# Kernel tuning notes

Measured on AMD Instinct MI355X. Metric: run time of the kernel, lower is better.

Reference implementation:

```python
import jax, jax.numpy as jnp
import numpy as np
import math

B, T, C, H, RANK, RD = 8, 512, 2048, 16, 8, 16
HD = C // H  # 128
ADAPTER_SCALE = 1.0 / RANK  # scale / rank with scale=1.0


def setup_inputs() -> dict:
    key = jax.random.key(0)
    ks = jax.random.split(key, 7)
    x = jax.random.normal(ks[0], (B, T, C), dtype=jnp.float32)
    # frozen random linears (weights ~ N(0,1)/sqrt(in_features))
    Wqkv = jax.random.normal(ks[1], (3 * C, C), dtype=jnp.float32) / math.sqrt(C)
    Wout = jax.random.normal(ks[2], (C, C), dtype=jnp.float32) / math.sqrt(C)
    # VeRA frozen random matrices
    A0_qkv = jax.random.normal(ks[3], (RANK, C), dtype=jnp.float32) / math.sqrt(C)
    B0_qkv = jax.random.normal(ks[4], (3 * C, RANK), dtype=jnp.float32) / math.sqrt(RANK)
    A0_out = jax.random.normal(ks[5], (RANK, C), dtype=jnp.float32) / math.sqrt(C)
    B0_out = jax.random.normal(ks[6], (C, RANK), dtype=jnp.float32) / math.sqrt(RANK)
    # learned scaling vectors (init to ones, as in the module)
    d_a_qkv = jnp.ones((RANK,), dtype=jnp.float32)
    d_b_qkv = jnp.ones((RANK,), dtype=jnp.float32)
    d_a_out = jnp.ones((RANK,), dtype=jnp.float32)
    d_b_out = jnp.ones((RANK,), dtype=jnp.float32)
    # partial RoPE caches over first RD dims
    freqs = 1.0 / (10000.0 ** (jnp.arange(0, RD, 2, dtype=jnp.float32) / RD))  # [RD/2]
    ang = jnp.arange(T, dtype=jnp.float32)[:, None] * freqs[None, :]  # [T, RD/2]
    cos = jnp.cos(ang)
    sin = jnp.sin(ang)
    return {"x": x, "Wqkv": Wqkv, "A0_qkv": A0_qkv, "B0_qkv": B0_qkv,
            "d_a_qkv": d_a_qkv, "d_b_qkv": d_b_qkv,
            "Wout": Wout, "A0_out": A0_out, "B0_out": B0_out,
            "d_a_out": d_a_out, "d_b_out": d_b_out,
            "cos": cos, "sin": sin}


def _adapted_linear(x, W, A0, B0, d_a, d_b):
    # frozen(x) + VeRA adapter: diag(d_b) B0 diag(d_a) A0, scaled by 1/rank
    base = x @ W.T
    h = (x @ A0.T) * (d_a * d_b)
    return base + (h @ B0.T) * ADAPTER_SCALE


def _apply_rope(q, cos, sin):
    # q: [B, H, T, HD]; rotate first RD dims, pass-through the rest
    x_rope, x_pass = q[..., :RD], q[..., RD:]
    half = RD // 2
    x1, x2 = x_rope[..., :half], x_rope[..., half:]
    c = cos[None, None]  # [1,1,T,RD/2]
    s = sin[None, None]
    rot = jnp.concatenate([x1 * c - x2 * s, x2 * c + x1 * s], axis=-1)
    return jnp.concatenate([rot, x_pass], axis=-1)


def reference(x, Wqkv, A0_qkv, B0_qkv, d_a_qkv, d_b_qkv,
              Wout, A0_out, B0_out, d_a_out, d_b_out, cos, sin):
    qkv = _adapted_linear(x, Wqkv, A0_qkv, B0_qkv, d_a_qkv, d_b_qkv)  # [B,T,3C]
    qkv = qkv.reshape(B, T, 3, H, HD)
    q = jnp.transpose(qkv[:, :, 0], (0, 2, 1, 3))  # [B,H,T,HD]
    k = jnp.transpose(qkv[:, :, 1], (0, 2, 1, 3))
    v = jnp.transpose(qkv[:, :, 2], (0, 2, 1, 3))
    q = _apply_rope(q, cos, sin)
    k = _apply_rope(k, cos, sin)
    # causal SDPA
    scale = 1.0 / math.sqrt(HD)
    scores = jnp.einsum('bhqd,bhkd->bhqk', q, k) * scale
    mask = jnp.tril(jnp.ones((T, T), dtype=bool))
    scores = jnp.where(mask[None, None], scores, jnp.finfo(scores.dtype).min)
    attn = jax.nn.softmax(scores, axis=-1)
    y = jnp.einsum('bhqk,bhkd->bhqd', attn, v)  # [B,H,T,HD]
    y = jnp.transpose(y, (0, 2, 1, 3)).reshape(B, T, C)
    return _adapted_linear(y, Wout, A0_out, B0_out, d_a_out, d_b_out)
```

## Files before the change

kernel.cpp:

```cpp
#include <hip/hip_runtime.h>

typedef unsigned short ushort_t;
typedef __attribute__((ext_vector_type(8))) short short8;
typedef __attribute__((ext_vector_type(4))) float f32x4;

#define AS1(p) ((const __attribute__((address_space(1))) void*)(p))
#define AS3(p) ((__attribute__((address_space(3))) void*)(p))

__device__ __forceinline__ ushort_t f2bf(float f){
  unsigned u = __float_as_uint(f);
  u += 0x7FFFu + ((u>>16)&1u);
  return (ushort_t)(u>>16);
}
__device__ __forceinline__ float bf2f(ushort_t h){
  return __uint_as_float(((unsigned)h)<<16);
}

__global__ __launch_bounds__(256) void conv_f2b(const float* __restrict__ src,
                                                ushort_t* __restrict__ dst, int n){
  int i = (blockIdx.x*256 + threadIdx.x)*4;
  if (i < n){
    float4 v = *(const float4*)&src[i];
    ushort_t o0=f2bf(v.x), o1=f2bf(v.y), o2=f2bf(v.z), o3=f2bf(v.w);
    ushort4 o; o.x=o0; o.y=o1; o.z=o2; o.w=o3;
    *(ushort4*)&dst[i] = o;
  }
}

__global__ __launch_bounds__(256) void lora_h_f32(const float* __restrict__ X,
                                                  ushort_t* __restrict__ Xbf,
                                                  const float* __restrict__ A0,
                                                  const float* __restrict__ da,
                                                  const float* __restrict__ db,
                                                  float* __restrict__ out, int K){
  int m = blockIdx.x;
  int tid = threadIdx.x, lane = tid & 63, w = tid >> 6;
  float part[8] = {0,0,0,0,0,0,0,0};
  for (int k = tid; k < K; k += 256){
    float xv = X[(size_t)m*K + k];
    Xbf[(size_t)m*K + k] = f2bf(xv);
    #pragma unroll
    for (int r=0;r<8;++r) part[r] += xv * A0[r*K + k];
  }
  #pragma unroll
  for (int r=0;r<8;++r)
    for (int d=1;d<64;d<<=1) part[r] += __shfl_xor(part[r], d, 64);
  __shared__ float wsum[4][8];
  if (lane==0){
    #pragma unroll
    for (int r=0;r<8;++r) wsum[w][r] = part[r];
  }
  __syncthreads();
  if (tid < 8){
    float s = wsum[0][tid]+wsum[1][tid]+wsum[2][tid]+wsum[3][tid];
    out[(size_t)m*8 + tid] = s * da[tid]*db[tid];
  }
}

__global__ __launch_bounds__(256) void lora_h_bf16(const ushort_t* __restrict__ X,
                                                   const float* __restrict__ A0,
                                                   const float* __restrict__ da,
                                                   const float* __restrict__ db,
                                                   float* __restrict__ out, int K){
  int m = blockIdx.x;
  int tid = threadIdx.x, lane = tid & 63, w = tid >> 6;
  float part[8] = {0,0,0,0,0,0,0,0};
  for (int k = tid; k < K; k += 256){
    float xv = bf2f(X[(size_t)m*K + k]);
    #pragma unroll
    for (int r=0;r<8;++r) part[r] += xv * A0[r*K + k];
  }
  #pragma unroll
  for (int r=0;r<8;++r)
    for (int d=1;d<64;d<<=1) part[r] += __shfl_xor(part[r], d, 64);
  __shared__ float wsum[4][8];
  if (lane==0){
    #pragma unroll
    for (int r=0;r<8;++r) wsum[w][r] = part[r];
  }
  __syncthreads();
  if (tid < 8){
    float s = wsum[0][tid]+wsum[1][tid]+wsum[2][tid]+wsum[3][tid];
    out[(size_t)m*8 + tid] = s * da[tid]*db[tid];
  }
}

__global__ __launch_bounds__(512, 1) void gemm256x192_lora(
    const ushort_t* __restrict__ A, const ushort_t* __restrict__ Bw,
    const float* __restrict__ hmat, const float* __restrict__ B0,
    ushort_t* __restrict__ C, int M, int N, int K)
{
  __shared__ __align__(16) char smem[114688];
  const int tid = threadIdx.x, lane = tid & 63, w = tid >> 6;
  const int wm = w >> 1, wn = w & 1;

  const int nbn = N / 192;
  const int nwg = (M >> 8) * nbn;
  const int q8 = nwg >> 3;
  const int swz = ((int)blockIdx.x & 7)*q8 + ((int)blockIdx.x >> 3);
  const int m0 = (swz / nbn) << 8, n0 = (swz % nbn) * 192;

  const int NTt = K >> 6;
  const int srow8  = tid >> 3;
  const int schunk = (lane & 7) ^ (lane >> 3);

  #define STAGE_AU(u, tt, bb) do { \
    const ushort_t* g_ = A + (size_t)(m0 + (u)*64 + srow8)*K + (tt)*64 + schunk*8; \
    __builtin_amdgcn_global_load_lds(AS1(g_), AS3(smem + (bb)*32768 + (u)*8192 + tid*16), 16, 0, 0); \
  } while(0)
  #define STAGE_BU(u, tt, bb) do { \
    const ushort_t* g_ = Bw + (size_t)(n0 + (u)*64 + srow8)*K + (tt)*64 + schunk*8; \
    __builtin_amdgcn_global_load_lds(AS1(g_), AS3(smem + 65536 + (bb)*24576 + (u)*8192 + tid*16), 16, 0, 0); \
  } while(0)

  #define RDA(bb, q, kk) (*(const short8*)(smem + (bb)*32768 + \
      ((q)*64 + wm*16 + (lane&15))*128 + ((((kk)*4 + (lane>>4)) ^ (lane&7))<<4)))
  #define RDB(bb, r, kk) (*(const short8*)(smem + 65536 + (bb)*24576 + \
      ((r)*32 + wn*16 + (lane&15))*128 + ((((kk)*4 + (lane>>4)) ^ (lane&7))<<4)))

  #define MM(q, r, bi) do{ \
    acc[q][r] = __builtin_amdgcn_mfma_f32_16x16x32_bf16(aF[q][0], bF[bi][0], acc[q][r], 0,0,0); \
    acc[q][r] = __builtin_amdgcn_mfma_f32_16x16x32_bf16(aF[q][1], bF[bi][1], acc[q][r], 0,0,0); \
  }while(0)

  #define BARRIER() asm volatile("s_barrier" ::: "memory")

  short8 aF[4][2];
  short8 bF[2][2];
  f32x4 acc[4][6] = {};

  STAGE_AU(0,0,0); STAGE_AU(1,0,0); STAGE_AU(2,0,0); STAGE_AU(3,0,0);
  STAGE_BU(0,0,0); STAGE_BU(1,0,0); STAGE_BU(2,0,0);
  asm volatile("s_waitcnt vmcnt(2)" ::: "memory");
  BARRIER();

  for (int t = 0; t < NTt-1; ++t){
    const int b = t & 1, nb = b ^ 1;
    #pragma unroll
    for (int q=0;q<4;++q){ aF[q][0]=RDA(b,q,0); aF[q][1]=RDA(b,q,1); }
    #pragma unroll
    for (int rl=0;rl<2;++rl){ bF[rl][0]=RDB(b,rl,0); bF[rl][1]=RDB(b,rl,1); }
    STAGE_AU(0,t+1,nb); STAGE_AU(1,t+1,nb);
    __builtin_amdgcn_s_setprio(1);
    MM(0,0,0); MM(0,1,1); MM(1,0,0); MM(1,1,1);
    MM(2,0,0); MM(2,1,1); MM(3,0,0); MM(3,1,1);
    __builtin_amdgcn_s_setprio(0);
    asm volatile("s_waitcnt vmcnt(3)" ::: "memory");
    BARRIER();
    #pragma unroll
    for (int rl=0;rl<2;++rl){ bF[rl][0]=RDB(b,rl+2,0); bF[rl][1]=RDB(b,rl+2,1); }
    STAGE_AU(2,t+1,nb); STAGE_AU(3,t+1,nb); STAGE_BU(0,t+1,nb);
    __builtin_amdgcn_s_setprio(1);
    MM(0,2,0); MM(0,3,1); MM(1,2,0); MM(1,3,1);
    MM(2,2,0); MM(2,3,1); MM(3,2,0); MM(3,3,1);
    __builtin_amdgcn_s_setprio(0);
    asm volatile("s_waitcnt vmcnt(5)" ::: "memory");
    BARRIER();
    #pragma unroll
    for (int rl=0;rl<2;++rl){ bF[rl][0]=RDB(b,rl+4,0); bF[rl][1]=RDB(b,rl+4,1); }
    STAGE_BU(1,t+1,nb); STAGE_BU(2,t+1,nb);
    __builtin_amdgcn_s_setprio(1);
    MM(0,4,0); MM(0,5,1); MM(1,4,0); MM(1,5,1);
    MM(2,4,0); MM(2,5,1); MM(3,4,0); MM(3,5,1);
    __builtin_amdgcn_s_setprio(0);
    asm volatile("s_waitcnt lgkmcnt(0)" ::: "memory");
    asm volatile("s_waitcnt vmcnt(2)" ::: "memory");
    BARRIER();
  }

  {
    const int b = (NTt-1) & 1;
    #pragma unroll
    for (int q=0;q<4;++q){ aF[q][0]=RDA(b,q,0); aF[q][1]=RDA(b,q,1); }
    #pragma unroll
    for (int rl=0;rl<2;++rl){ bF[rl][0]=RDB(b,rl,0); bF[rl][1]=RDB(b,rl,1); }
    __builtin_amdgcn_s_setprio(1);
    MM(0,0,0); MM(0,1,1); MM(1,0,0); MM(1,1,1);
    MM(2,0,0); MM(2,1,1); MM(3,0,0); MM(3,1,1);
    __builtin_amdgcn_s_setprio(0);
    asm volatile("s_waitcnt vmcnt(1)" ::: "memory");
    BARRIER();
    #pragma unroll
    for (int rl=0;rl<2;++rl){ bF[rl][0]=RDB(b,rl+2,0); bF[rl][1]=RDB(b,rl+2,1); }
    __builtin_amdgcn_s_setprio(1);
    MM(0,2,0); MM(0,3,1); MM(1,2,0); MM(1,3,1);
    MM(2,2,0); MM(2,3,1); MM(3,2,0); MM(3,3,1);
    __builtin_amdgcn_s_setprio(0);
    asm volatile("s_waitcnt vmcnt(0)" ::: "memory");
    BARRIER();
    #pragma unroll
    for (int rl=0;rl<2;++rl){ bF[rl][0]=RDB(b,rl+4,0); bF[rl][1]=RDB(b,rl+4,1); }
    MM(0,4,0); MM(0,5,1); MM(1,4,0); MM(1,5,1);
    MM(2,4,0); MM(2,5,1); MM(3,4,0); MM(3,5,1);
  }

  float b0v[6][8];
  #pragma unroll
  for (int r=0;r<6;++r){
    int col = n0 + r*32 + wn*16 + (lane&15);
    const float4* bp = (const float4*)&B0[(size_t)col*8];
    float4 u0 = bp[0], u1 = bp[1];
    b0v[r][0]=u0.x; b0v[r][1]=u0.y; b0v[r][2]=u0.z; b0v[r][3]=u0.w;
    b0v[r][4]=u1.x; b0v[r][5]=u1.y; b0v[r][6]=u1.z; b0v[r][7]=u1.w;
  }
  #pragma unroll
  for (int q=0;q<4;++q){
    #pragma unroll
    for (int jj=0;jj<4;++jj){
      int row = m0 + q*64 + wm*16 + (lane>>4)*4 + jj;
      const float4* hp = (const float4*)&hmat[(size_t)row*8];
      float4 h0 = hp[0], h1 = hp[1];
      #pragma unroll
      for (int r=0;r<6;++r){
        float lor = h0.x*b0v[r][0]+h0.y*b0v[r][1]+h0.z*b0v[r][2]+h0.w*b0v[r][3]
                  + h1.x*b0v[r][4]+h1.y*b0v[r][5]+h1.z*b0v[r][6]+h1.w*b0v[r][7];
        int col = n0 + r*32 + wn*16 + (lane&15);
        C[(size_t)row*N + col] = f2bf(acc[q][r][jj] + 0.125f*lor);
      }
    }
  }
  #undef STAGE_AU
  #undef STAGE_BU
  #undef RDA
  #undef RDB
  #undef MM
  #undef BARRIER
}

template<int MODE>
__global__ __launch_bounds__(512, 1) void gemm128x256_lora(
    const ushort_t* __restrict__ A, const ushort_t* __restrict__ Bw,
    const float* __restrict__ hmat, const float* __restrict__ B0,
    void* __restrict__ C, int M, int N, int K)
{
  __shared__ __align__(16) char smem[98304];
  const int tid = threadIdx.x, lane = tid & 63, w = tid >> 6;
  const int wm = w >> 2, wn = w & 3;

  const int nbn = N >> 8;
  const int nwg = (M >> 7) * nbn;
  const int q8 = nwg >> 3;
  const int swz = ((int)blockIdx.x & 7)*q8 + ((int)blockIdx.x >> 3);
  const int m0 = (swz / nbn) << 7, n0 = (swz % nbn) << 8;

  const int NTt = K >> 6;

  const int srow8  = tid >> 3;
  const int schunk = (lane & 7) ^ (lane >> 3);

  #define STAGE_AU(u, tt, bb) do { \
    const ushort_t* g_ = A + (size_t)(m0 + (u)*64 + srow8)*K + (tt)*64 + schunk*8; \
    __builtin_amdgcn_global_load_lds(AS1(g_), AS3(smem + (bb)*16384 + (u)*8192 + w*1024), 16, 0, 0); \
  } while(0)
  #define STAGE_BU(u, tt, bb) do { \
    const ushort_t* g_ = Bw + (size_t)(n0 + (u)*64 + srow8)*K + (tt)*64 + schunk*8; \
    __builtin_amdgcn_global_load_lds(AS1(g_), AS3(smem + 32768 + (bb)*32768 + (u)*8192 + w*1024), 16, 0, 0); \
  } while(0)

  #define RDA(bb, q, kk) (*(const short8*)(smem + (bb)*16384 + \
      ((q)*32 + wm*16 + (lane&15))*128 + ((((kk)*4 + (lane>>4)) ^ (lane&7))<<4)))
  #define RDB(bb, rg, kk) (*(const short8*)(smem + 32768 + (bb)*32768 + \
      ((rg)*64 + wn*16 + (lane&15))*128 + ((((kk)*4 + (lane>>4)) ^ (lane&7))<<4)))

  #define MM0(q,rl) do{ \
    acc[q][rl] = __builtin_amdgcn_mfma_f32_16x16x32_bf16(aF[q][0], bF[rl][0], acc[q][rl], 0,0,0); \
    acc[q][rl] = __builtin_amdgcn_mfma_f32_16x16x32_bf16(aF[q][1], bF[rl][1], acc[q][rl], 0,0,0); \
  }while(0)
  #define MM1(q,rl) do{ \
    acc[q][(rl)+2] = __builtin_amdgcn_mfma_f32_16x16x32_bf16(aF[q][0], bF[rl][0], acc[q][(rl)+2], 0,0,0); \
    acc[q][(rl)+2] = __builtin_amdgcn_mfma_f32_16x16x32_bf16(aF[q][1], bF[rl][1], acc[q][(rl)+2], 0,0,0); \
  }while(0)

  #define BARRIER() asm volatile("s_barrier" ::: "memory")

  short8 aF[4][2];
  short8 bF[2][2];
  f32x4 acc[4][4] = {};

  STAGE_AU(0,0,0); STAGE_AU(1,0,0); STAGE_BU(0,0,0); STAGE_BU(1,0,0);
  STAGE_BU(2,0,0); STAGE_BU(3,0,0);
  asm volatile("s_waitcnt vmcnt(2)" ::: "memory");
  BARRIER();

  for (int t = 0; t < NTt-1; ++t){
    const int b = t & 1, nb = b ^ 1;
    #pragma unroll
    for (int q=0;q<4;++q){ aF[q][0]=RDA(b,q,0); aF[q][1]=RDA(b,q,1); }
    #pragma unroll
    for (int rl=0;rl<2;++rl){ bF[rl][0]=RDB(b,rl,0); bF[rl][1]=RDB(b,rl,1); }
    STAGE_AU(0,t+1,nb); STAGE_AU(1,t+1,nb); STAGE_BU(0,t+1,nb); STAGE_BU(1,t+1,nb);
    __builtin_amdgcn_s_setprio(1);
    MM0(0,0); MM0(0,1); MM0(1,0); MM0(1,1);
    MM0(2,0); MM0(2,1); MM0(3,0); MM0(3,1);
    __builtin_amdgcn_s_setprio(0);
    asm volatile("s_waitcnt vmcnt(4)" ::: "memory");
    BARRIER();
    #pragma unroll
    for (int rl=0;rl<2;++rl){ bF[rl][0]=RDB(b,rl+2,0); bF[rl][1]=RDB(b,rl+2,1); }
    STAGE_BU(2,t+1,nb); STAGE_BU(3,t+1,nb);
    __builtin_amdgcn_s_setprio(1);
    MM1(0,0); MM1(0,1); MM1(1,0); MM1(1,1);
    MM1(2,0); MM1(2,1); MM1(3,0); MM1(3,1);
    __builtin_amdgcn_s_setprio(0);
    asm volatile("s_waitcnt lgkmcnt(0)" ::: "memory");
    asm volatile("s_waitcnt vmcnt(2)" ::: "memory");
    BARRIER();
  }

  {
    const int b = (NTt-1) & 1;
    #pragma unroll
    for (int q=0;q<4;++q){ aF[q][0]=RDA(b,q,0); aF[q][1]=RDA(b,q,1); }
    #pragma unroll
    for (int rl=0;rl<2;++rl){ bF[rl][0]=RDB(b,rl,0); bF[rl][1]=RDB(b,rl,1); }
    __builtin_amdgcn_s_setprio(1);
    MM0(0,0); MM0(0,1); MM0(1,0); MM0(1,1);
    MM0(2,0); MM0(2,1); MM0(3,0); MM0(3,1);
    __builtin_amdgcn_s_setprio(0);
    asm volatile("s_waitcnt vmcnt(0)" ::: "memory");
    BARRIER();
    #pragma unroll
    for (int rl=0;rl<2;++rl){ bF[rl][0]=RDB(b,rl+2,0); bF[rl][1]=RDB(b,rl+2,1); }
    MM1(0,0); MM1(0,1); MM1(1,0); MM1(1,1);
    MM1(2,0); MM1(2,1); MM1(3,0); MM1(3,1);
  }

  float b0v[4][8];
  #pragma unroll
  for (int r=0;r<4;++r){
    int col = n0 + r*64 + wn*16 + (lane&15);
    const float4* bp = (const float4*)&B0[(size_t)col*8];
    float4 u0 = bp[0], u1 = bp[1];
    b0v[r][0]=u0.x; b0v[r][1]=u0.y; b0v[r][2]=u0.z; b0v[r][3]=u0.w;
    b0v[r][4]=u1.x; b0v[r][5]=u1.y; b0v[r][6]=u1.z; b0v[r][7]=u1.w;
  }
  #pragma unroll
  for (int q=0;q<4;++q){
    #pragma unroll
    for (int jj=0;jj<4;++jj){
      int row = m0 + q*32 + wm*16 + (lane>>4)*4 + jj;
      const float4* hp = (const float4*)&hmat[(size_t)row*8];
      float4 h0 = hp[0], h1 = hp[1];
      #pragma unroll
      for (int r=0;r<4;++r){
        float lor = h0.x*b0v[r][0]+h0.y*b0v[r][1]+h0.z*b0v[r][2]+h0.w*b0v[r][3]
                  + h1.x*b0v[r][4]+h1.y*b0v[r][5]+h1.z*b0v[r][6]+h1.w*b0v[r][7];
        int col = n0 + r*64 + wn*16 + (lane&15);
        float v = acc[q][r][jj] + 0.125f*lor;
        if (MODE==0) ((ushort_t*)C)[(size_t)row*N + col] = f2bf(v);
        else         ((float*)C)[(size_t)row*N + col]    = v;
      }
    }
  }
  #undef STAGE_AU
  #undef STAGE_BU
  #undef RDA
  #undef RDB
  #undef MM0
  #undef MM1
  #undef BARRIER
}

__global__ __launch_bounds__(256) void rope_kernel(ushort_t* __restrict__ qkv,
                                                   const float* __restrict__ cosb,
                                                   const float* __restrict__ sinb){
  int idx = blockIdx.x*256 + threadIdx.x;
  int d = idx & 7;
  int g = idx >> 3;
  int h_ = g & 15;
  int s  = (g>>4) & 1;
  int t  = (g>>5) & 511;
  int b  = g >> 14;
  size_t base = (size_t)(b*512 + t)*6144 + s*2048 + h_*128;
  float x1 = bf2f(qkv[base+d]), x2 = bf2f(qkv[base+d+8]);
  float c = cosb[t*8+d], sn = sinb[t*8+d];
  qkv[base+d]   = f2bf(x1*c - x2*sn);
  qkv[base+d+8] = f2bf(x2*c + x1*sn);
}

__global__ __launch_bounds__(256) void attn_kernel(const ushort_t* __restrict__ qkv,
                                                   ushort_t* __restrict__ y){
  __shared__ __align__(16) ushort_t Ks[64*128];
  __shared__ __align__(16) ushort_t Vt[128*64];
  __shared__ __align__(16) ushort_t Pl[4][16*64];

  const int qt = blockIdx.x, hh = blockIdx.y, b = blockIdx.z;
  const int tid = threadIdx.x, lane = tid & 63, w = tid >> 6, g = lane >> 4;
  const int qb0 = qt*64;
  const int row_base = b*512;
  const int qoff = hh*128;
  const int koff = 2048 + hh*128;
  const int voff = 4096 + hh*128;
  const float scale = 0.08838834764831845f;

  short8 qf[4];
  {
    int qr = qb0 + w*16 + (lane & 15);
    const ushort_t* qp = qkv + (size_t)(row_base + qr)*6144 + qoff + g*8;
    #pragma unroll
    for (int kc=0;kc<4;++kc) qf[kc] = *(const short8*)(qp + kc*32);
  }

  const int krow = tid >> 4;
  const int kc_  = tid & 15;
  const int kcs  = (kc_ & 8) | ((kc_ ^ (krow & 7)) & 7);
  const int vr   = tid >> 2;
  const int vd0  = (tid & 3) * 32;
  const int vrhi = vr >> 3, vrlo = vr & 7;

  f32x4 o[8] = {};
  float mrow[4] = {-1e30f,-1e30f,-1e30f,-1e30f};
  float lrow[4] = {0,0,0,0};

  for (int t = 0; t <= qt; ++t){
    const int kv0 = t*64;
    __syncthreads();
    {
      const ushort_t* kg = qkv + (size_t)(row_base + kv0 + krow)*6144 + koff + kcs*8;
      #pragma unroll
      for (int i=0;i<4;++i)
        __builtin_amdgcn_global_load_lds(AS1(kg + (size_t)(i*16)*6144),
                                         AS3((char*)Ks + i*4096 + tid*16), 16, 0, 0);
    }
    {
      const ushort_t* vg = qkv + (size_t)(row_base + kv0 + vr)*6144 + voff + vd0;
      short8 vv0 = ((const short8*)vg)[0];
      short8 vv1 = ((const short8*)vg)[1];
      short8 vv2 = ((const short8*)vg)[2];
      short8 vv3 = ((const short8*)vg)[3];
      #pragma unroll
      for (int ii=0;ii<8;++ii){
        int sw = (vrhi ^ ii) << 3;
        Vt[(vd0 + ii     )*64 + sw + vrlo] = (ushort_t)vv0[ii];
        Vt[(vd0 + 8 + ii )*64 + sw + vrlo] = (ushort_t)vv1[ii];
        Vt[(vd0 + 16 + ii)*64 + sw + vrlo] = (ushort_t)vv2[ii];
        Vt[(vd0 + 24 + ii)*64 + sw + vrlo] = (ushort_t)vv3[ii];
      }
    }
    __syncthreads();

    f32x4 s4[4] = {};
    #pragma unroll
    for (int cg=0;cg<4;++cg){
      const int row = cg*16 + (lane&15);
      const int rx = row & 7;
      #pragma unroll
      for (int kc=0;kc<4;++kc){
        const int ch = kc*4 + g;
        const short8 kfv = *(const short8*)&Ks[row*128 + (((ch&8)|((ch^rx)&7))<<3)];
        s4[cg] = __builtin_amdgcn_mfma_f32_16x16x32_bf16(qf[kc], kfv, s4[cg], 0, 0, 0);
      }
    }

    const bool diag = (t == qt);
    float fac[4], p0[4], p1[4], p2[4], p3[4];
    #pragma unroll
    for (int j=0;j<4;++j){
      float a0 = s4[0][j]*scale, a1 = s4[1][j]*scale, a2 = s4[2][j]*scale, a3 = s4[3][j]*scale;
      if (diag){
        int q_abs = qb0 + w*16 + g*4 + j;
        int c0 = kv0 + (lane&15);
        if (c0      > q_abs) a0 = -1e30f;
        if (c0 + 16 > q_abs) a1 = -1e30f;
        if (c0 + 32 > q_abs) a2 = -1e30f;
        if (c0 + 48 > q_abs) a3 = -1e30f;
      }
      float mx = fmaxf(fmaxf(a0,a1), fmaxf(a2,a3));
      #pragma unroll
      for (int d=1; d<16; d<<=1) mx = fmaxf(mx, __shfl_xor(mx, d, 16));
      float mn = fmaxf(mrow[j], mx);
      float f  = __expf(mrow[j] - mn);
      mrow[j] = mn; fac[j] = f;
      p0[j] = __expf(a0 - mn); p1[j] = __expf(a1 - mn);
      p2[j] = __expf(a2 - mn); p3[j] = __expf(a3 - mn);
      float rs = p0[j] + p1[j] + p2[j] + p3[j];
      #pragma unroll
      for (int d=1; d<16; d<<=1) rs += __shfl_xor(rs, d, 16);
      lrow[j] = lrow[j]*f + rs;
    }
    #pragma unroll
    for (int n=0;n<8;++n){
      #pragma unroll
      for (int j=0;j<4;++j) o[n][j] *= fac[j];
    }

    {
      ushort_t* plw = &Pl[w][0];
      #pragma unroll
      for (int j=0;j<4;++j){
        const int prow = g*4 + j;
        const int rx = prow & 7;
        const int cl = (lane&15)>>3, c7 = lane&7;
        plw[prow*64 + (((0*2+cl)^rx)<<3) + c7] = f2bf(p0[j]);
        plw[prow*64 + (((1*2+cl)^rx)<<3) + c7] = f2bf(p1[j]);
        plw[prow*64 + (((2*2+cl)^rx)<<3) + c7] = f2bf(p2[j]);
        plw[prow*64 + (((3*2+cl)^rx)<<3) + c7] = f2bf(p3[j]);
      }
    }
    {
      const ushort_t* plw = &Pl[w][0];
      const int rowP = lane & 15, rxp = rowP & 7;
      const short8 pf0 = *(const short8*)&plw[rowP*64 + (((g  )^rxp)<<3)];
      const short8 pf1 = *(const short8*)&plw[rowP*64 + (((4+g)^rxp)<<3)];
      #pragma unroll
      for (int n=0;n<8;++n){
        const int d = n*16 + (lane&15);
        const int dx = d & 7;
        const short8 vf0 = *(const short8*)&Vt[d*64 + (((g  )^dx)<<3)];
        const short8 vf1 = *(const short8*)&Vt[d*64 + (((4+g)^dx)<<3)];
        o[n] = __builtin_amdgcn_mfma_f32_16x16x32_bf16(pf0, vf0, o[n], 0, 0, 0);
        o[n] = __builtin_amdgcn_mfma_f32_16x16x32_bf16(pf1, vf1, o[n], 0, 0, 0);
      }
    }
  }

  #pragma unroll
  for (int j=0;j<4;++j){
    float inv = 1.0f / lrow[j];
    int qr = qb0 + w*16 + g*4 + j;
    #pragma unroll
    for (int n=0;n<8;++n)
      y[(size_t)(row_base+qr)*2048 + hh*128 + n*16 + (lane&15)] = f2bf(o[n][j]*inv);
  }
}

extern "C" void kernel_launch(void* const* d_in, const int* in_sizes, int n_in,
                              void* d_out, int out_size, void* d_ws, size_t ws_size,
                              hipStream_t stream){
  const float* x       = (const float*)d_in[0];
  const float* Wqkv    = (const float*)d_in[1];
  const float* A0_qkv  = (const float*)d_in[2];
  const float* B0_qkv  = (const float*)d_in[3];
  const float* da_qkv  = (const float*)d_in[4];
  const float* db_qkv  = (const float*)d_in[5];
  const float* Wout    = (const float*)d_in[6];
  const float* A0_out  = (const float*)d_in[7];
  const float* B0_out  = (const float*)d_in[8];
  const float* da_out  = (const float*)d_in[9];
  const float* db_out  = (const float*)d_in[10];
  const float* cosb    = (const float*)d_in[11];
  const float* sinb    = (const float*)d_in[12];
  float* out = (float*)d_out;

  char* ws = (char*)d_ws;
  ushort_t* x_bf    = (ushort_t*)(ws);
  ushort_t* wqkv_bf = (ushort_t*)(ws + 16777216);
  ushort_t* wout_bf = (ushort_t*)(ws + 41943040);
  ushort_t* qkv_bf  = (ushort_t*)(ws + 50331648);
  ushort_t* y_bf    = (ushort_t*)(ws + 100663296);
  float*    h_qkv   = (float*)   (ws + 117440512);
  float*    h_out   = (float*)   (ws + 117571584);

  const int M = 4096;
  const int C = 2048;
  const int N3 = 6144;

  conv_f2b<<<12288,256, 0, stream>>>(Wqkv, wqkv_bf, N3*C);
  conv_f2b<<<4096, 256, 0, stream>>>(Wout, wout_bf, C*C);

  lora_h_f32<<<M, 256, 0, stream>>>(x, x_bf, A0_qkv, da_qkv, db_qkv, h_qkv, C);

  gemm256x192_lora<<<(M/256)*(N3/192), 512, 0, stream>>>(x_bf, wqkv_bf, h_qkv, B0_qkv,
                                                         qkv_bf, M, N3, C);

  rope_kernel<<<4096, 256, 0, stream>>>(qkv_bf, cosb, sinb);

  attn_kernel<<<dim3(8, 16, 8), 256, 0, stream>>>(qkv_bf, y_bf);

  lora_h_bf16<<<M, 256, 0, stream>>>(y_bf, A0_out, da_out, db_out, h_out, C);

  gemm128x256_lora<1><<<(M/128)*(C/256), 512, 0, stream>>>(y_bf, wout_bf, h_out, B0_out,
                                                           out, M, C, C);
}
```

Measured before the change: 251.5 us.

## Double-buffer K/V tiles and use 128-query blocks with 8 waves in attention

The attention kernel now processes 128 query rows per block with 512 threads (8 waves), so each K/V tile loaded into shared memory is reused by twice as many queries. K and V tiles are double-buffered: the next tile's global loads are issued before computing on the current one, and a single barrier per iteration replaces two. Waves whose query rows lie entirely above a KV tile skip that tile's compute. This doubles LDS usage and halves the grid to 512 blocks, which may reduce occupancy and worsen load balance across the causal triangle.

```diff
diff --git a/kernel.cpp b/kernel.cpp
--- a/kernel.cpp
+++ b/kernel.cpp
@@ -378,15 +378,15 @@
   qkv[base+d+8] = f2bf(x2*c + x1*sn);
 }
 
-__global__ __launch_bounds__(256) void attn_kernel(const ushort_t* __restrict__ qkv,
+__global__ __launch_bounds__(512) void attn_kernel(const ushort_t* __restrict__ qkv,
                                                    ushort_t* __restrict__ y){
-  __shared__ __align__(16) ushort_t Ks[64*128];
-  __shared__ __align__(16) ushort_t Vt[128*64];
-  __shared__ __align__(16) ushort_t Pl[4][16*64];
+  __shared__ __align__(16) ushort_t Ks[2][64*128];
+  __shared__ __align__(16) ushort_t Vt[2][128*64];
+  __shared__ __align__(16) ushort_t Pl[8][16*64];
 
   const int qt = blockIdx.x, hh = blockIdx.y, b = blockIdx.z;
   const int tid = threadIdx.x, lane = tid & 63, w = tid >> 6, g = lane >> 4;
-  const int qb0 = qt*64;
+  const int qb0 = qt*128;
   const int row_base = b*512;
   const int qoff = hh*128;
   const int koff = 2048 + hh*128;
@@ -404,114 +404,136 @@
   const int krow = tid >> 4;
   const int kc_  = tid & 15;
   const int kcs  = (kc_ & 8) | ((kc_ ^ (krow & 7)) & 7);
-  const int vr   = tid >> 2;
-  const int vd0  = (tid & 3) * 32;
+  const int vr   = tid >> 3;
+  const int vd0  = (tid & 7) * 16;
   const int vrhi = vr >> 3, vrlo = vr & 7;
+
+  const int nt = 2*qt + 2;
+  const int wmin = qb0 + w*16;
+  const int wmax = wmin + 15;
 
   f32x4 o[8] = {};
   float mrow[4] = {-1e30f,-1e30f,-1e30f,-1e30f};
   float lrow[4] = {0,0,0,0};
 
-  for (int t = 0; t <= qt; ++t){
+  short8 vv0, vv1;
+
+  {
+    const ushort_t* kg = qkv + (size_t)(row_base + krow)*6144 + koff + kcs*8;
+    __builtin_amdgcn_global_load_lds(AS1(kg), AS3((char*)&Ks[0][0] + tid*16), 16, 0, 0);
+    __builtin_amdgcn_global_load_lds(AS1(kg + (size_t)32*6144), AS3((char*)&Ks[0][0] + 8192 + tid*16), 16, 0, 0);
+    const ushort_t* vg = qkv + (size_t)(row_base + vr)*6144 + voff + vd0;
+    vv0 = ((const short8*)vg)[0];
+    vv1 = ((const short8*)vg)[1];
+    #pragma unroll
+    for (int ii=0;ii<8;++ii){
+      int sw = (vrhi ^ ii) << 3;
+      Vt[0][(vd0 + ii    )*64 + sw + vrlo] = (ushort_t)vv0[ii];
+      Vt[0][(vd0 + 8 + ii)*64 + sw + vrlo] = (ushort_t)vv1[ii];
+    }
+  }
+  __syncthreads();
+
+  for (int t = 0; t < nt; ++t){
+    const int bb = t & 1, nb = bb ^ 1;
     const int kv0 = t*64;
-    __syncthreads();
-    {
-      const ushort_t* kg = qkv + (size_t)(row_base + kv0 + krow)*6144 + koff + kcs*8;
+    const bool have_next = (t+1 < nt);
+
+    if (have_next){
+      const int kv1 = kv0 + 64;
+      const ushort_t* kg = qkv + (size_t)(row_base + kv1 + krow)*6144 + koff + kcs*8;
+      __builtin_amdgcn_global_load_lds(AS1(kg), AS3((char*)&Ks[nb][0] + tid*16), 16, 0, 0);
+      __builtin_amdgcn_global_load_lds(AS1(kg + (size_t)32*6144), AS3((char*)&Ks[nb][0] + 8192 + tid*16), 16, 0, 0);
+      const ushort_t* vg = qkv + (size_t)(row_base + kv1 + vr)*6144 + voff + vd0;
+      vv0 = ((const short8*)vg)[0];
+      vv1 = ((const short8*)vg)[1];
+    }
+
+    if (kv0 <= wmax){
+      f32x4 s4[4] = {};
       #pragma unroll
-      for (int i=0;i<4;++i)
-        __builtin_amdgcn_global_load_lds(AS1(kg + (size_t)(i*16)*6144),
-                                         AS3((char*)Ks + i*4096 + tid*16), 16, 0, 0);
+      for (int cg=0;cg<4;++cg){
+        const int row = cg*16 + (lane&15);
+        const int rx = row & 7;
+        #pragma unroll
+        for (int kc=0;kc<4;++kc){
+          const int ch = kc*4 + g;
+          const short8 kfv = *(const short8*)&Ks[bb][row*128 + (((ch&8)|((ch^rx)&7))<<3)];
+          s4[cg] = __builtin_amdgcn_mfma_f32_16x16x32_bf16(qf[kc], kfv, s4[cg], 0, 0, 0);
+        }
+      }
+
+      const bool diag = (kv0 + 63 > wmin);
+      float fac[4], p0[4], p1[4], p2[4], p3[4];
+      #pragma unroll
+      for (int j=0;j<4;++j){
+        float a0 = s4[0][j]*scale, a1 = s4[1][j]*scale, a2 = s4[2][j]*scale, a3 = s4[3][j]*scale;
+        if (diag){
+          int q_abs = wmin + g*4 + j;
+          int c0 = kv0 + (lane&15);
+          if (c0      > q_abs) a0 = -1e30f;
+          if (c0 + 16 > q_abs) a1 = -1e30f;
+          if (c0 + 32 > q_abs) a2 = -1e30f;
+          if (c0 + 48 > q_abs) a3 = -1e30f;
+        }
+        float mx = fmaxf(fmaxf(a0,a1), fmaxf(a2,a3));
+        #pragma unroll
+        for (int d=1; d<16; d<<=1) mx = fmaxf(mx, __shfl_xor(mx, d, 16));
+        float mn = fmaxf(mrow[j], mx);
+        float f  = __expf(mrow[j] - mn);
+        mrow[j] = mn; fac[j] = f;
+        p0[j] = __expf(a0 - mn); p1[j] = __expf(a1 - mn);
+        p2[j] = __expf(a2 - mn); p3[j] = __expf(a3 - mn);
+        float rs = p0[j] + p1[j] + p2[j] + p3[j];
+        #pragma unroll
+        for (int d=1; d<16; d<<=1) rs += __shfl_xor(rs, d, 16);
+        lrow[j] = lrow[j]*f + rs;
+      }
+      #pragma unroll
+      for (int n=0;n<8;++n){
+        #pragma unroll
+        for (int j=0;j<4;++j) o[n][j] *= fac[j];
+      }
+
+      {
+        ushort_t* plw = &Pl[w][0];
+        #pragma unroll
+        for (int j=0;j<4;++j){
+          const int prow = g*4 + j;
+          const int rx = prow & 7;
+          const int cl = (lane&15)>>3, c7 = lane&7;
+          plw[prow*64 + (((0*2+cl)^rx)<<3) + c7] = f2bf(p0[j]);
+          plw[prow*64 + (((1*2+cl)^rx)<<3) + c7] = f2bf(p1[j]);
+          plw[prow*64 + (((2*2+cl)^rx)<<3) + c7] = f2bf(p2[j]);
+          plw[prow*64 + (((3*2+cl)^rx)<<3) + c7] = f2bf(p3[j]);
+        }
+      }
+      {
+        const ushort_t* plw = &Pl[w][0];
+        const int rowP = lane & 15, rxp = rowP & 7;
+        const short8 pf0 = *(const short8*)&plw[rowP*64 + (((g  )^rxp)<<3)];
+        const short8 pf1 = *(const short8*)&plw[rowP*64 + (((4+g)^rxp)<<3)];
+        #pragma unroll
+        for (int n=0;n<8;++n){
+          const int d = n*16 + (lane&15);
+          const int dx = d & 7;
+          const short8 vf0 = *(const short8*)&Vt[bb][d*64 + (((g  )^dx)<<3)];
+          const short8 vf1 = *(const short8*)&Vt[bb][d*64 + (((4+g)^dx)<<3)];
+          o[n] = __builtin_amdgcn_mfma_f32_16x16x32_bf16(pf0, vf0, o[n], 0, 0, 0);
+          o[n] = __builtin_amdgcn_mfma_f32_16x16x32_bf16(pf1, vf1, o[n], 0, 0, 0);
+        }
+      }
     }
-    {
-      const ushort_t* vg = qkv + (size_t)(row_base + kv0 + vr)*6144 + voff + vd0;
-      short8 vv0 = ((const short8*)vg)[0];
-      short8 vv1 = ((const short8*)vg)[1];
-      short8 vv2 = ((const short8*)vg)[2];
-      short8 vv3 = ((const short8*)vg)[3];
+
+    if (have_next){
       #pragma unroll
       for (int ii=0;ii<8;++ii){
         int sw = (vrhi ^ ii) << 3;
-        Vt[(vd0 + ii     )*64 + sw + vrlo] = (ushort_t)vv0[ii];
-        Vt[(vd0 + 8 + ii )*64 + sw + vrlo] = (ushort_t)vv1[ii];
-        Vt[(vd0 + 16 + ii)*64 + sw + vrlo] = (ushort_t)vv2[ii];
-        Vt[(vd0 + 24 + ii)*64 + sw + vrlo] = (ushort_t)vv3[ii];
+        Vt[nb][(vd0 + ii    )*64 + sw + vrlo] = (ushort_t)vv0[ii];
+        Vt[nb][(vd0 + 8 + ii)*64 + sw + vrlo] = (ushort_t)vv1[ii];
       }
     }
     __syncthreads();
-
-    f32x4 s4[4] = {};
-    #pragma unroll
-    for (int cg=0;cg<4;++cg){
-      const int row = cg*16 + (lane&15);
-      const int rx = row & 7;
-      #pragma unroll
-      for (int kc=0;kc<4;++kc){
-        const int ch = kc*4 + g;
-        const short8 kfv = *(const short8*)&Ks[row*128 + (((ch&8)|((ch^rx)&7))<<3)];
-        s4[cg] = __builtin_amdgcn_mfma_f32_16x16x32_bf16(qf[kc], kfv, s4[cg], 0, 0, 0);
-      }
-    }
-
-    const bool diag = (t == qt);
-    float fac[4], p0[4], p1[4], p2[4], p3[4];
-    #pragma unroll
-    for (int j=0;j<4;++j){
-      float a0 = s4[0][j]*scale, a1 = s4[1][j]*scale, a2 = s4[2][j]*scale, a3 = s4[3][j]*scale;
-      if (diag){
-        int q_abs = qb0 + w*16 + g*4 + j;
-        int c0 = kv0 + (lane&15);
-        if (c0      > q_abs) a0 = -1e30f;
-        if (c0 + 16 > q_abs) a1 = -1e30f;
-        if (c0 + 32 > q_abs) a2 = -1e30f;
-        if (c0 + 48 > q_abs) a3 = -1e30f;
-      }
-      float mx = fmaxf(fmaxf(a0,a1), fmaxf(a2,a3));
-      #pragma unroll
-      for (int d=1; d<16; d<<=1) mx = fmaxf(mx, __shfl_xor(mx, d, 16));
-      float mn = fmaxf(mrow[j], mx);
-      float f  = __expf(mrow[j] - mn);
-      mrow[j] = mn; fac[j] = f;
-      p0[j] = __expf(a0 - mn); p1[j] = __expf(a1 - mn);
-      p2[j] = __expf(a2 - mn); p3[j] = __expf(a3 - mn);
-      float rs = p0[j] + p1[j] + p2[j] + p3[j];
-      #pragma unroll
-      for (int d=1; d<16; d<<=1) rs += __shfl_xor(rs, d, 16);
-      lrow[j] = lrow[j]*f + rs;
-    }
-    #pragma unroll
-    for (int n=0;n<8;++n){
-      #pragma unroll
-      for (int j=0;j<4;++j) o[n][j] *= fac[j];
-    }
-
-    {
-      ushort_t* plw = &Pl[w][0];
-      #pragma unroll
-      for (int j=0;j<4;++j){
-        const int prow = g*4 + j;
-        const int rx = prow & 7;
-        const int cl = (lane&15)>>3, c7 = lane&7;
-        plw[prow*64 + (((0*2+cl)^rx)<<3) + c7] = f2bf(p0[j]);
-        plw[prow*64 + (((1*2+cl)^rx)<<3) + c7] = f2bf(p1[j]);
-        plw[prow*64 + (((2*2+cl)^rx)<<3) + c7] = f2bf(p2[j]);
-        plw[prow*64 + (((3*2+cl)^rx)<<3) + c7] = f2bf(p3[j]);
-      }
-    }
-    {
-      const ushort_t* plw = &Pl[w][0];
-      const int rowP = lane & 15, rxp = rowP & 7;
-      const short8 pf0 = *(const short8*)&plw[rowP*64 + (((g  )^rxp)<<3)];
-      const short8 pf1 = *(const short8*)&plw[rowP*64 + (((4+g)^rxp)<<3)];
-      #pragma unroll
-      for (int n=0;n<8;++n){
-        const int d = n*16 + (lane&15);
-        const int dx = d & 7;
-        const short8 vf0 = *(const short8*)&Vt[d*64 + (((g  )^dx)<<3)];
-        const short8 vf1 = *(const short8*)&Vt[d*64 + (((4+g)^dx)<<3)];
-        o[n] = __builtin_amdgcn_mfma_f32_16x16x32_bf16(pf0, vf0, o[n], 0, 0, 0);
-        o[n] = __builtin_amdgcn_mfma_f32_16x16x32_bf16(pf1, vf1, o[n], 0, 0, 0);
-      }
-    }
   }
 
   #pragma unroll
@@ -565,7 +587,7 @@
 
   rope_kernel<<<4096, 256, 0, stream>>>(qkv_bf, cosb, sinb);
 
-  attn_kernel<<<dim3(8, 16, 8), 256, 0, stream>>>(qkv_bf, y_bf);
+  attn_kernel<<<dim3(4, 16, 8), 512, 0, stream>>>(qkv_bf, y_bf);
 
   lora_h_bf16<<<M, 256, 0, stream>>>(y_bf, A0_out, da_out, db_out, h_out, C);
 
```

Measured after the change: 248.3 us. Within noise of the previous version (-1.3%).
